# Performance work log

Measured on AMD Instinct MI355X. Metric: run time of the kernel, lower is better.

Reference implementation:

```python
import jax, jax.numpy as jnp
import numpy as np

OUT_FEATURES = 4096
IN_FEATURES = 4096
BATCH = 2048
NNZ = 1_600_000


def setup_inputs() -> dict:
    key = jax.random.key(0)
    k1, k2, k3, k4, k5 = jax.random.split(key, 5)
    rows = jax.random.randint(k1, (NNZ,), 0, OUT_FEATURES, dtype=jnp.int32)
    cols = jax.random.randint(k2, (NNZ,), 0, IN_FEATURES, dtype=jnp.int32)
    values = jax.random.normal(k3, (NNZ,), dtype=jnp.float32) * 0.02
    bias = jax.random.normal(k4, (OUT_FEATURES, 1), dtype=jnp.float32) * 0.02
    inp = jax.random.normal(k5, (IN_FEATURES, BATCH), dtype=jnp.float32)
    return {"inp": inp, "values": values, "bias": bias, "rows": rows, "cols": cols}


def reference(inp, values, bias, rows, cols):
    # Sparse COO addmm: out = bias + W @ inp, W sparse [OUT, IN].
    # Scatter-add the COO triplets into a dense weight (sums duplicates,
    # matching coalesced-COO spmm semantics), then one dense GEMM.
    W = jnp.zeros((OUT_FEATURES, IN_FEATURES), dtype=values.dtype).at[rows, cols].add(values)
    return W @ inp + bias  # [OUT, BATCH], bias [OUT,1] broadcasts over batch
```

## Files before the change

kernel.cpp:

```cpp
#include <hip/hip_runtime.h>
#include <stdint.h>

#define OUTF 4096
#define INF  4096
#define NBAT 2048
#define BM 128
#define BN 128
#define BK 32

typedef __attribute__((ext_vector_type(8))) short bf16x8;
typedef __attribute__((ext_vector_type(4))) float f32x4;
typedef __attribute__((ext_vector_type(4))) unsigned int u32x4;

typedef const __attribute__((address_space(1))) uint8_t* gptr_t;
typedef __attribute__((address_space(3))) uint8_t* lptr_t;

__device__ __forceinline__ uint32_t f2bf(float f) {
  uint32_t u = __builtin_bit_cast(uint32_t, f);
  return (u + 0x7FFFu + ((u >> 16) & 1u)) >> 16;
}

__global__ void zeroW_kernel(uint4* __restrict__ W) {
  W[(size_t)blockIdx.x * 256 + threadIdx.x] = make_uint4(0u, 0u, 0u, 0u);
}

__global__ void scatter_kernel(const float* __restrict__ vals,
                               const int* __restrict__ rows,
                               const int* __restrict__ cols,
                               float* __restrict__ W, int nnz) {
  int i = blockIdx.x * blockDim.x + threadIdx.x;
  if (i < nnz) atomicAdd(&W[(size_t)rows[i] * INF + cols[i]], vals[i]);
}

__global__ void packW_kernel(uint32_t* __restrict__ W) {
  size_t i = ((size_t)blockIdx.x * 256 + threadIdx.x) * 4;
  uint4 p = *(const uint4*)(W + i);
  uint32_t o[4];
  uint32_t w[4] = {p.x, p.y, p.z, p.w};
#pragma unroll
  for (int j = 0; j < 4; ++j) {
    float f = __builtin_bit_cast(float, w[j]);
    uint32_t hi = f2bf(f);
    float fhi = __builtin_bit_cast(float, hi << 16);
    uint32_t lo = f2bf(f - fhi);
    o[j] = (hi << 16) | lo;
  }
  *(uint4*)(W + i) = make_uint4(o[0], o[1], o[2], o[3]);
}

__global__ void packX_kernel(const float* __restrict__ X,
                             uint16_t* __restrict__ Xh,
                             uint16_t* __restrict__ Xl) {
  __shared__ float t[32][33];
  int n0 = blockIdx.x * 32, k0 = blockIdx.y * 32;
  int tx = threadIdx.x, ty = threadIdx.y;
#pragma unroll
  for (int j = 0; j < 4; ++j)
    t[ty + j * 8][tx] = X[(size_t)(k0 + ty + j * 8) * NBAT + n0 + tx];
  __syncthreads();
#pragma unroll
  for (int j = 0; j < 4; ++j) {
    int n = n0 + ty + j * 8, k = k0 + tx;
    float f = t[tx][ty + j * 8];
    uint32_t hi = f2bf(f);
    float fhi = __builtin_bit_cast(float, hi << 16);
    uint32_t lo = f2bf(f - fhi);
    Xh[(size_t)n * INF + k] = (uint16_t)hi;
    Xl[(size_t)n * INF + k] = (uint16_t)lo;
  }
}

__global__ __launch_bounds__(256, 2) void gemm_kernel(
    const uint32_t* __restrict__ Wp,
    const uint16_t* __restrict__ Xh,
    const uint16_t* __restrict__ Xl,
    const float* __restrict__ bias,
    float* __restrict__ out) {
  __shared__ __align__(16) uint8_t lds[32768];
  uint8_t* la = lds;
  uint8_t* lb = lds + 16384;

  const unsigned tid = threadIdx.x;
  const unsigned lane = tid & 63, wid = tid >> 6;
  const unsigned wr = wid >> 1, wc = wid & 1;

  unsigned newid = (blockIdx.x & 7) * 64 + (blockIdx.x >> 3);
  const unsigned bm = newid & 31, bn = newid >> 5;

  const uint8_t* aSrc[4];
  const uint8_t* bSrc[4];
#pragma unroll
  for (int i = 0; i < 4; ++i) {
    unsigned d = i * 4096 + tid * 16;
    unsigned row = d >> 7;
    unsigned ch = (d >> 4) & 7;
    unsigned sc = ch ^ (row & 7);
    aSrc[i] = (const uint8_t*)Wp + (size_t)(bm * BM + row) * (INF * 4) + sc * 16;
    const uint16_t* base = (sc & 4) ? Xl : Xh;
    bSrc[i] = (const uint8_t*)(base + (size_t)(bn * BN + row) * INF + (sc & 3) * 8);
  }

  const unsigned kg = lane >> 4, lr = lane & 15;
  unsigned aOff[4][2], bOffH[4], bOffL[4];
#pragma unroll
  for (int mi = 0; mi < 4; ++mi) {
    unsigned row = wr * 64 + mi * 16 + lr;
    aOff[mi][0] = row * 128 + (((kg * 2 + 0) ^ (row & 7)) * 16);
    aOff[mi][1] = row * 128 + (((kg * 2 + 1) ^ (row & 7)) * 16);
  }
#pragma unroll
  for (int ni = 0; ni < 4; ++ni) {
    unsigned col = wc * 64 + ni * 16 + lr;
    bOffH[ni] = col * 128 + (((0 + kg) ^ (col & 7)) * 16);
    bOffL[ni] = col * 128 + (((4 + kg) ^ (col & 7)) * 16);
  }

  f32x4 acc[4][4] = {};

  for (unsigned kt = 0; kt < INF / BK; ++kt) {
#pragma unroll
    for (int i = 0; i < 4; ++i) {
      __builtin_amdgcn_global_load_lds((gptr_t)(aSrc[i] + (size_t)kt * 128),
                                       (lptr_t)(la + i * 4096 + wid * 1024), 16, 0, 0);
      __builtin_amdgcn_global_load_lds((gptr_t)(bSrc[i] + (size_t)kt * 64),
                                       (lptr_t)(lb + i * 4096 + wid * 1024), 16, 0, 0);
    }
    __syncthreads();

    bf16x8 ah[4], al[4], bh[4], bl[4];
#pragma unroll
    for (int mi = 0; mi < 4; ++mi) {
      uint4 p0 = *(const uint4*)(la + aOff[mi][0]);
      uint4 p1 = *(const uint4*)(la + aOff[mi][1]);
      u32x4 h, l;
      h[0] = (p0.x >> 16) | (p0.y & 0xFFFF0000u);  l[0] = (p0.x & 0xFFFFu) | (p0.y << 16);
      h[1] = (p0.z >> 16) | (p0.w & 0xFFFF0000u);  l[1] = (p0.z & 0xFFFFu) | (p0.w << 16);
      h[2] = (p1.x >> 16) | (p1.y & 0xFFFF0000u);  l[2] = (p1.x & 0xFFFFu) | (p1.y << 16);
      h[3] = (p1.z >> 16) | (p1.w & 0xFFFF0000u);  l[3] = (p1.z & 0xFFFFu) | (p1.w << 16);
      ah[mi] = __builtin_bit_cast(bf16x8, h);
      al[mi] = __builtin_bit_cast(bf16x8, l);
    }
#pragma unroll
    for (int ni = 0; ni < 4; ++ni) {
      bh[ni] = *(const bf16x8*)(lb + bOffH[ni]);
      bl[ni] = *(const bf16x8*)(lb + bOffL[ni]);
    }
#pragma unroll
    for (int mi = 0; mi < 4; ++mi)
#pragma unroll
      for (int ni = 0; ni < 4; ++ni) {
        acc[mi][ni] = __builtin_amdgcn_mfma_f32_16x16x32_bf16(ah[mi], bh[ni], acc[mi][ni], 0, 0, 0);
        acc[mi][ni] = __builtin_amdgcn_mfma_f32_16x16x32_bf16(ah[mi], bl[ni], acc[mi][ni], 0, 0, 0);
        acc[mi][ni] = __builtin_amdgcn_mfma_f32_16x16x32_bf16(al[mi], bh[ni], acc[mi][ni], 0, 0, 0);
      }
    __syncthreads();
  }

  const unsigned lq = lane >> 4;
#pragma unroll
  for (int mi = 0; mi < 4; ++mi) {
    unsigned row0 = bm * BM + wr * 64 + mi * 16 + lq * 4;
#pragma unroll
    for (int ni = 0; ni < 4; ++ni) {
      unsigned col = bn * BN + wc * 64 + ni * 16 + lr;
#pragma unroll
      for (int r = 0; r < 4; ++r)
        out[(size_t)(row0 + r) * NBAT + col] = acc[mi][ni][r] + bias[row0 + r];
    }
  }
}

extern "C" void kernel_launch(void* const* d_in, const int* in_sizes, int n_in,
                              void* d_out, int out_size, void* d_ws, size_t ws_size,
                              hipStream_t stream) {
  const float* inp    = (const float*)d_in[0];
  const float* values = (const float*)d_in[1];
  const float* bias   = (const float*)d_in[2];
  const int*   rows   = (const int*)d_in[3];
  const int*   cols   = (const int*)d_in[4];
  const int nnz = in_sizes[1];
  float* out = (float*)d_out;

  uint8_t* ws = (uint8_t*)d_ws;
  float*    W  = (float*)ws;
  uint16_t* Xh = (uint16_t*)(ws + (64u << 20));
  uint16_t* Xl = (uint16_t*)(ws + (80u << 20));

  zeroW_kernel<<<(OUTF * (size_t)INF * 4) / (256 * 16), 256, 0, stream>>>((uint4*)W);
  scatter_kernel<<<(nnz + 255) / 256, 256, 0, stream>>>(values, rows, cols, W, nnz);
  packW_kernel<<<(OUTF * (size_t)INF / 4) / 256, 256, 0, stream>>>((uint32_t*)W);
  packX_kernel<<<dim3(NBAT / 32, INF / 32), dim3(32, 8), 0, stream>>>(inp, Xh, Xl);
  gemm_kernel<<<(OUTF / BM) * (NBAT / BN), 256, 0, stream>>>(
      (const uint32_t*)W, Xh, Xl, bias, out);
}
```

Measured before the change: 391.0 us.

## Double-buffer GEMM LDS pipeline, split fp32 W in-kernel, fuse zero and X-pack

The GEMM now double-buffers its LDS tiles, issuing global-to-LDS loads two K-steps ahead with explicit vmcnt waits and raw barriers. This is meant to hide global load latency behind MFMA work. It reads the fp32 dense W directly and splits it into bf16 hi/lo pairs in registers. That removes the separate packW pass over the 64MB weight matrix, at the cost of extra ALU work per tile and a truncated rather than rounded low part. The W zeroing and X transposition/packing are merged into one launch, and MFMA sections are wrapped in s_setprio.

Result: no change. 390.4 us (-0.1%).

```diff
diff --git a/kernel.cpp b/kernel.cpp
--- a/kernel.cpp
+++ b/kernel.cpp
@@ -6,12 +6,10 @@
 #define NBAT 2048
 #define BM 128
 #define BN 128
-#define BK 32
 
 typedef __attribute__((ext_vector_type(8))) short bf16x8;
 typedef __attribute__((ext_vector_type(4))) float f32x4;
 typedef __attribute__((ext_vector_type(4))) unsigned int u32x4;
-
 typedef const __attribute__((address_space(1))) uint8_t* gptr_t;
 typedef __attribute__((address_space(3))) uint8_t* lptr_t;
 
@@ -20,40 +18,28 @@
   return (u + 0x7FFFu + ((u >> 16) & 1u)) >> 16;
 }
 
-__global__ void zeroW_kernel(uint4* __restrict__ W) {
-  W[(size_t)blockIdx.x * 256 + threadIdx.x] = make_uint4(0u, 0u, 0u, 0u);
-}
-
-__global__ void scatter_kernel(const float* __restrict__ vals,
-                               const int* __restrict__ rows,
-                               const int* __restrict__ cols,
-                               float* __restrict__ W, int nnz) {
-  int i = blockIdx.x * blockDim.x + threadIdx.x;
-  if (i < nnz) atomicAdd(&W[(size_t)rows[i] * INF + cols[i]], vals[i]);
-}
-
-__global__ void packW_kernel(uint32_t* __restrict__ W) {
-  size_t i = ((size_t)blockIdx.x * 256 + threadIdx.x) * 4;
-  uint4 p = *(const uint4*)(W + i);
-  uint32_t o[4];
-  uint32_t w[4] = {p.x, p.y, p.z, p.w};
-#pragma unroll
-  for (int j = 0; j < 4; ++j) {
-    float f = __builtin_bit_cast(float, w[j]);
-    uint32_t hi = f2bf(f);
-    float fhi = __builtin_bit_cast(float, hi << 16);
-    uint32_t lo = f2bf(f - fhi);
-    o[j] = (hi << 16) | lo;
-  }
-  *(uint4*)(W + i) = make_uint4(o[0], o[1], o[2], o[3]);
-}
-
-__global__ void packX_kernel(const float* __restrict__ X,
-                             uint16_t* __restrict__ Xh,
-                             uint16_t* __restrict__ Xl) {
+__device__ __forceinline__ void split2(uint32_t u0, uint32_t u1,
+                                       uint32_t& h, uint32_t& l) {
+  uint32_t h0 = (u0 + 0x7FFFu + ((u0 >> 16) & 1u)) >> 16;
+  uint32_t h1 = (u1 + 0x7FFFu + ((u1 >> 16) & 1u)) >> 16;
+  float r0 = __builtin_bit_cast(float, u0) - __builtin_bit_cast(float, h0 << 16);
+  float r1 = __builtin_bit_cast(float, u1) - __builtin_bit_cast(float, h1 << 16);
+  h = h0 | (h1 << 16);
+  l = (__builtin_bit_cast(uint32_t, r0) >> 16) |
+      (__builtin_bit_cast(uint32_t, r1) & 0xFFFF0000u);
+}
+
+__global__ void zero_packX_kernel(uint4* __restrict__ W, const float* __restrict__ X,
+                                  uint16_t* __restrict__ Xh, uint16_t* __restrict__ Xl) {
+  unsigned bid = blockIdx.x;
+  if (bid < 16384) {
+    W[(size_t)bid * 256 + threadIdx.x] = make_uint4(0u, 0u, 0u, 0u);
+    return;
+  }
+  bid -= 16384;
   __shared__ float t[32][33];
-  int n0 = blockIdx.x * 32, k0 = blockIdx.y * 32;
-  int tx = threadIdx.x, ty = threadIdx.y;
+  int n0 = (bid & 63) * 32, k0 = (bid >> 6) * 32;
+  int tx = threadIdx.x & 31, ty = threadIdx.x >> 5;
 #pragma unroll
   for (int j = 0; j < 4; ++j)
     t[ty + j * 8][tx] = X[(size_t)(k0 + ty + j * 8) * NBAT + n0 + tx];
@@ -70,15 +56,34 @@
   }
 }
 
+__global__ void scatter_kernel(const float* __restrict__ vals,
+                               const int* __restrict__ rows,
+                               const int* __restrict__ cols,
+                               float* __restrict__ W, int nnz) {
+  int i = blockIdx.x * blockDim.x + threadIdx.x;
+  if (i < nnz) atomicAdd(&W[(size_t)rows[i] * INF + cols[i]], vals[i]);
+}
+
+#define WAIT_VM(N) do { asm volatile("s_waitcnt vmcnt(" #N ")" ::: "memory"); } while (0)
+#define BAR __builtin_amdgcn_s_barrier()
+
+#define STAGE(BS) do { \
+  _Pragma("unroll") for (int i = 0; i < 4; ++i) { \
+    __builtin_amdgcn_global_load_lds((gptr_t)aSrc[i], \
+        (lptr_t)(lds + (BS) * 32768 + i * 4096 + wid * 1024), 16, 0, 0); \
+    aSrc[i] += 128; \
+    __builtin_amdgcn_global_load_lds((gptr_t)bSrc[i], \
+        (lptr_t)(lds + (BS) * 32768 + 16384 + i * 4096 + wid * 1024), 16, 0, 0); \
+    bSrc[i] += 64; } \
+} while (0)
+
 __global__ __launch_bounds__(256, 2) void gemm_kernel(
-    const uint32_t* __restrict__ Wp,
+    const float* __restrict__ Wr,
     const uint16_t* __restrict__ Xh,
     const uint16_t* __restrict__ Xl,
     const float* __restrict__ bias,
     float* __restrict__ out) {
-  __shared__ __align__(16) uint8_t lds[32768];
-  uint8_t* la = lds;
-  uint8_t* lb = lds + 16384;
+  __shared__ __align__(16) uint8_t lds[65536];
 
   const unsigned tid = threadIdx.x;
   const unsigned lane = tid & 63, wid = tid >> 6;
@@ -95,7 +100,7 @@
     unsigned row = d >> 7;
     unsigned ch = (d >> 4) & 7;
     unsigned sc = ch ^ (row & 7);
-    aSrc[i] = (const uint8_t*)Wp + (size_t)(bm * BM + row) * (INF * 4) + sc * 16;
+    aSrc[i] = (const uint8_t*)Wr + (size_t)(bm * BM + row) * (INF * 4) + sc * 16;
     const uint16_t* base = (sc & 4) ? Xl : Xh;
     bSrc[i] = (const uint8_t*)(base + (size_t)(bn * BN + row) * INF + (sc & 3) * 8);
   }
@@ -117,34 +122,36 @@
 
   f32x4 acc[4][4] = {};
 
-  for (unsigned kt = 0; kt < INF / BK; ++kt) {
-#pragma unroll
-    for (int i = 0; i < 4; ++i) {
-      __builtin_amdgcn_global_load_lds((gptr_t)(aSrc[i] + (size_t)kt * 128),
-                                       (lptr_t)(la + i * 4096 + wid * 1024), 16, 0, 0);
-      __builtin_amdgcn_global_load_lds((gptr_t)(bSrc[i] + (size_t)kt * 64),
-                                       (lptr_t)(lb + i * 4096 + wid * 1024), 16, 0, 0);
-    }
-    __syncthreads();
+  STAGE(0);
+  STAGE(1);
+  WAIT_VM(8);
+  BAR;
+  __builtin_amdgcn_sched_barrier(0);
+
+  for (int t = 0; t < 128; ++t) {
+    const unsigned bo = (t & 1) * 32768;
 
     bf16x8 ah[4], al[4], bh[4], bl[4];
 #pragma unroll
     for (int mi = 0; mi < 4; ++mi) {
-      uint4 p0 = *(const uint4*)(la + aOff[mi][0]);
-      uint4 p1 = *(const uint4*)(la + aOff[mi][1]);
+      uint4 p0 = *(const uint4*)(lds + bo + aOff[mi][0]);
+      uint4 p1 = *(const uint4*)(lds + bo + aOff[mi][1]);
       u32x4 h, l;
-      h[0] = (p0.x >> 16) | (p0.y & 0xFFFF0000u);  l[0] = (p0.x & 0xFFFFu) | (p0.y << 16);
-      h[1] = (p0.z >> 16) | (p0.w & 0xFFFF0000u);  l[1] = (p0.z & 0xFFFFu) | (p0.w << 16);
-      h[2] = (p1.x >> 16) | (p1.y & 0xFFFF0000u);  l[2] = (p1.x & 0xFFFFu) | (p1.y << 16);
-      h[3] = (p1.z >> 16) | (p1.w & 0xFFFF0000u);  l[3] = (p1.z & 0xFFFFu) | (p1.w << 16);
+      uint32_t th, tl;
+      split2(p0.x, p0.y, th, tl); h[0] = th; l[0] = tl;
+      split2(p0.z, p0.w, th, tl); h[1] = th; l[1] = tl;
+      split2(p1.x, p1.y, th, tl); h[2] = th; l[2] = tl;
+      split2(p1.z, p1.w, th, tl); h[3] = th; l[3] = tl;
       ah[mi] = __builtin_bit_cast(bf16x8, h);
       al[mi] = __builtin_bit_cast(bf16x8, l);
     }
 #pragma unroll
     for (int ni = 0; ni < 4; ++ni) {
-      bh[ni] = *(const bf16x8*)(lb + bOffH[ni]);
-      bl[ni] = *(const bf16x8*)(lb + bOffL[ni]);
-    }
+      bh[ni] = *(const bf16x8*)(lds + bo + 16384 + bOffH[ni]);
+      bl[ni] = *(const bf16x8*)(lds + bo + 16384 + bOffL[ni]);
+    }
+
+    __builtin_amdgcn_s_setprio(1);
 #pragma unroll
     for (int mi = 0; mi < 4; ++mi)
 #pragma unroll
@@ -153,7 +160,19 @@
         acc[mi][ni] = __builtin_amdgcn_mfma_f32_16x16x32_bf16(ah[mi], bl[ni], acc[mi][ni], 0, 0, 0);
         acc[mi][ni] = __builtin_amdgcn_mfma_f32_16x16x32_bf16(al[mi], bh[ni], acc[mi][ni], 0, 0, 0);
       }
-    __syncthreads();
+    __builtin_amdgcn_s_setprio(0);
+
+    BAR;
+    if (t < 126) {
+      STAGE(t & 1);
+      WAIT_VM(8);
+    } else if (t == 126) {
+      WAIT_VM(0);
+    }
+    if (t < 127) {
+      BAR;
+      __builtin_amdgcn_sched_barrier(0);
+    }
   }
 
   const unsigned lq = lane >> 4;
@@ -186,10 +205,7 @@
   uint16_t* Xh = (uint16_t*)(ws + (64u << 20));
   uint16_t* Xl = (uint16_t*)(ws + (80u << 20));
 
-  zeroW_kernel<<<(OUTF * (size_t)INF * 4) / (256 * 16), 256, 0, stream>>>((uint4*)W);
+  zero_packX_kernel<<<16384 + 8192, 256, 0, stream>>>((uint4*)W, inp, Xh, Xl);
   scatter_kernel<<<(nnz + 255) / 256, 256, 0, stream>>>(values, rows, cols, W, nnz);
-  packW_kernel<<<(OUTF * (size_t)INF / 4) / 256, 256, 0, stream>>>((uint32_t*)W);
-  packX_kernel<<<dim3(NBAT / 32, INF / 32), dim3(32, 8), 0, stream>>>(inp, Xh, Xl);
-  gemm_kernel<<<(OUTF / BM) * (NBAT / BN), 256, 0, stream>>>(
-      (const uint32_t*)W, Xh, Xl, bias, out);
-}
+  gemm_kernel<<<512, 256, 0, stream>>>(W, Xh, Xl, bias, out);
+}
```
